# Performance work log

Measured on AMD Instinct MI355X. Metric: run time of the kernel, lower is better.

The kernel has to match this reference:

```python
import jax, jax.numpy as jnp
import numpy as np
from jax import lax

STRIDE = 16
SCALE = 16.0
ANCHOR_DIMS = (1.0, 2.0, 4.0, 8.0, 16.0, 32.0)
PRE_NMS_TOP_N = 6000
POST_NMS_TOP_N = 300
NMS_THRESH = 0.7


def conv2d(x, w, b, pad):
    y = lax.conv_general_dilated(x, w, (1, 1), [(pad, pad), (pad, pad)],
                                 dimension_numbers=("NCHW", "OIHW", "NCHW"))
    return y + b[None, :, None, None]


def setup_inputs() -> dict:
    key = jax.random.key(0)
    ks = jax.random.split(key, 6)
    B, C, H, W = 1, 1024, 128, 128
    A = len(ANCHOR_DIMS)
    return {
        "base_features": jax.random.normal(ks[0], (B, C, H, W), jnp.float32),
        "image_metadata": jnp.array([[H * STRIDE, W * STRIDE, 1.0]], jnp.float32),
        "gt_boxes": jax.random.uniform(ks[1], (B, 20, 5), jnp.float32) * 100.0,
        "W_conv": jax.random.normal(ks[2], (512, C, 3, 3), jnp.float32) / np.sqrt(C * 9.0),
        "b_conv": jnp.zeros((512,), jnp.float32),
        "W_cls": jax.random.normal(ks[3], (A, 512, 1, 1), jnp.float32) / np.sqrt(512.0),
        "b_cls": jnp.zeros((A,), jnp.float32),
        "W_bbox": jax.random.normal(ks[4], (4 * A, 512, 1, 1), jnp.float32) * 0.01,
        "b_bbox": jnp.zeros((4 * A,), jnp.float32),
    }


def _make_anchors(H, W):
    # square anchors of size dim*scale, centered on each feature cell
    dims = jnp.asarray(ANCHOR_DIMS, jnp.float32) * SCALE          # [A]
    cy = (jnp.arange(H, dtype=jnp.float32) + 0.5) * STRIDE        # [H]
    cx = (jnp.arange(W, dtype=jnp.float32) + 0.5) * STRIDE        # [W]
    half = 0.5 * dims[None, None, :]                              # [1,1,A]
    CX = cx[None, :, None]
    CY = cy[:, None, None]
    anchors = jnp.stack(jnp.broadcast_arrays(CX - half, CY - half, CX + half, CY + half), axis=-1)
    return anchors.reshape(-1, 4)                                 # [(H*W*A),4], order (h,w,a)


def _nms_fixed(boxes, scores):
    # boxes [N,4] already sorted by score desc; greedy NMS, POST_NMS_TOP_N picks
    x1, y1, x2, y2 = boxes[:, 0], boxes[:, 1], boxes[:, 2], boxes[:, 3]
    areas = jnp.maximum(x2 - x1, 0.0) * jnp.maximum(y2 - y1, 0.0)

    def body(i, state):
        alive, keep = state
        masked = jnp.where(alive, scores, -jnp.inf)
        j = jnp.argmax(masked)
        valid = masked[j] > -jnp.inf
        keep = keep.at[i].set(jnp.where(valid, j, -1).astype(jnp.int32))
        bj = boxes[j]
        iw = jnp.maximum(jnp.minimum(x2, bj[2]) - jnp.maximum(x1, bj[0]), 0.0)
        ih = jnp.maximum(jnp.minimum(y2, bj[3]) - jnp.maximum(y1, bj[1]), 0.0)
        inter = iw * ih
        iou = inter / (areas + areas[j] - inter + 1e-9)
        alive = alive & (iou <= NMS_THRESH)
        return alive, keep

    alive0 = jnp.ones(boxes.shape[0], bool)
    keep0 = jnp.full((POST_NMS_TOP_N,), -1, jnp.int32)
    _, keep = lax.fori_loop(0, POST_NMS_TOP_N, body, (alive0, keep0))
    return keep


def _proposal(prob, bbox, image_metadata):
    # original layer operates on detached tensors (.data)
    prob = lax.stop_gradient(prob)
    bbox = lax.stop_gradient(bbox)
    B, A, H, W = prob.shape
    anchors = _make_anchors(H, W)                                 # [N,4]
    scores = prob[0].transpose(1, 2, 0).reshape(-1)               # (h,w,a)
    deltas = bbox[0].reshape(A, 4, H, W).transpose(2, 3, 0, 1).reshape(-1, 4)
    wa = anchors[:, 2] - anchors[:, 0]
    ha = anchors[:, 3] - anchors[:, 1]
    cxa = anchors[:, 0] + 0.5 * wa
    cya = anchors[:, 1] + 0.5 * ha
    pcx = deltas[:, 0] * wa + cxa
    pcy = deltas[:, 1] * ha + cya
    pw = jnp.exp(deltas[:, 2]) * wa
    ph = jnp.exp(deltas[:, 3]) * ha
    boxes = jnp.stack([pcx - 0.5 * pw, pcy - 0.5 * ph, pcx + 0.5 * pw, pcy + 0.5 * ph], axis=1)
    im_h, im_w = image_metadata[0, 0], image_metadata[0, 1]
    boxes = jnp.stack([
        jnp.clip(boxes[:, 0], 0.0, im_w), jnp.clip(boxes[:, 1], 0.0, im_h),
        jnp.clip(boxes[:, 2], 0.0, im_w), jnp.clip(boxes[:, 3], 0.0, im_h)], axis=1)
    top_scores, top_idx = lax.top_k(scores, PRE_NMS_TOP_N)
    top_boxes = boxes[top_idx]
    keep = _nms_fixed(top_boxes, top_scores)
    sel = jnp.where(keep >= 0, keep, 0)
    kept = top_boxes[sel] * (keep >= 0).astype(top_boxes.dtype)[:, None]
    rois = jnp.concatenate([jnp.zeros((POST_NMS_TOP_N, 1), top_boxes.dtype), kept], axis=1)
    return rois                                                   # [POST_NMS_TOP_N, 5]


def reference(base_features, image_metadata, gt_boxes, W_conv, b_conv, W_cls, b_cls, W_bbox, b_bbox):
    conv1 = jax.nn.relu(conv2d(base_features, W_conv, b_conv, pad=1))   # [B,512,H,W]
    score = conv2d(conv1, W_cls, b_cls, pad=0)                          # [B,A,H,W]
    B, A, H, W = score.shape
    s2 = score.reshape(B, 2, (A * H) // 2, W)                           # RPN.reshape(x, 2)
    prob = jax.nn.softmax(s2, axis=1).reshape(B, A, H, W)               # reshape back to A channels
    bbox = conv2d(conv1, W_bbox, b_bbox, pad=0)                         # [B,4A,H,W]
    rois = _proposal(prob, bbox, image_metadata)
    return rois, prob, bbox
```

## Files before the change

### kernel.cpp

```cpp
#include <hip/hip_runtime.h>
#include <math.h>

typedef unsigned int u32;
typedef unsigned long long u64;
typedef short s16x8 __attribute__((ext_vector_type(8)));
typedef float f32x4 __attribute__((ext_vector_type(4)));

#define HH 128
#define WW 128
#define NPIX (128*128)
#define NANCH (NPIX*6)
#define KPRE 6000
#define KPOST 300
#define SORT_CAP 16384
#define RW 96
#define NMS_T 0.7f

#define OUT_PROB 1500
#define OUT_BBOX (1500 + 98304)

#define WS_CONV1 ((size_t)0)
#define WS_XTH   ((size_t)33554432)
#define WS_WPH   ((size_t)100663296)
#define WS_BOXES ((size_t)33554432)
#define WS_SCORE (WS_BOXES + 1572864)
#define WS_KEYS  (WS_SCORE + 393216)
#define WS_TB    (WS_KEYS + 131072)
#define WS_AREA  (WS_TB + 98304)
#define WS_SUP   (WS_AREA + 24576)
#define WS_HIST  (WS_SUP + 4718592)
#define WS_CTRL  (WS_HIST + 262144)
#define WS_KEEP  (WS_CTRL + 256)
#define WS_SKEYS (WS_KEEP + 1280)

__device__ __forceinline__ unsigned short f2bf(float x) {
    u32 b = __float_as_uint(x);
    u32 r = (b + 0x7FFFu + ((b >> 16) & 1u)) >> 16;
    return (unsigned short)r;
}

__device__ __forceinline__ void gl_lds16(const void* g, void* l) {
    __builtin_amdgcn_global_load_lds(
        (__attribute__((address_space(1))) const void*)g,
        (__attribute__((address_space(3))) void*)l,
        16, 0, 0);
}

__global__ void k_init(u32* __restrict__ hist, u32* __restrict__ ctrl,
                       int* __restrict__ keep, u64* __restrict__ keys) {
    int t = blockIdx.x * blockDim.x + threadIdx.x;
    if (t < 65536) hist[t] = 0u;
    if (t < 64)    ctrl[t] = 0u;
    if (t < 304)   keep[t] = -1;
    if (t < SORT_CAP) keys[t] = ~0ULL;
}

__global__ __launch_bounds__(256) void k_xsplit(const float* __restrict__ in,
                                                unsigned short* __restrict__ xth) {
    unsigned short* xtl = xth + 16777216;
    __shared__ unsigned short Th[64][72];
    __shared__ unsigned short Tl[64][72];
    const int px0 = blockIdx.x * 64;
    const int c0  = blockIdx.y * 64;
    const int t = threadIdx.x;
    const int r = t >> 4;
    const int p4 = (t & 15) * 4;
#pragma unroll
    for (int i = 0; i < 4; ++i) {
        int cr = r + 16 * i;
        float4 v = *(const float4*)(in + (size_t)(c0 + cr) * NPIX + px0 + p4);
        float vv[4] = {v.x, v.y, v.z, v.w};
#pragma unroll
        for (int k = 0; k < 4; ++k) {
            unsigned short h = f2bf(vv[k]);
            float hf = __uint_as_float((u32)h << 16);
            unsigned short l = f2bf(vv[k] - hf);
            Th[p4 + k][cr] = h;
            Tl[p4 + k][cr] = l;
        }
    }
    __syncthreads();
    const int p = t >> 2, q = t & 3;
    unsigned short* dh = xth + (size_t)(px0 + p) * 1024 + c0 + q * 16;
    unsigned short* dl = xtl + (size_t)(px0 + p) * 1024 + c0 + q * 16;
    *(uint4*)dh       = *(const uint4*)&Th[p][q * 16];
    *(uint4*)(dh + 8) = *(const uint4*)&Th[p][q * 16 + 8];
    *(uint4*)dl       = *(const uint4*)&Tl[p][q * 16];
    *(uint4*)(dl + 8) = *(const uint4*)&Tl[p][q * 16 + 8];
}

__global__ __launch_bounds__(256) void k_wpack(const float* __restrict__ w,
                                               unsigned short* __restrict__ wph,
                                               float* __restrict__ zstash) {
    if (blockIdx.x == 0 && threadIdx.x < 128) zstash[threadIdx.x] = 0.f;
    int id = blockIdx.x * 256 + threadIdx.x;
    int oc = id >> 10, c = id & 1023;
    const float* src = w + (size_t)oc * 9216 + c * 9;
#pragma unroll
    for (int tap = 0; tap < 9; ++tap) {
        float x = src[tap];
        unsigned short h = f2bf(x);
        unsigned short l = f2bf(x - __uint_as_float((u32)h << 16));
        wph[(size_t)tap * 524288 + id] = h;
        wph[4718592 + (size_t)tap * 524288 + id] = l;
    }
}

__global__ __launch_bounds__(256, 2) void k_conv3m(const unsigned short* __restrict__ xt,
                                                   const unsigned short* __restrict__ wp,
                                                   const float* __restrict__ bias,
                                                   const unsigned short* __restrict__ zst,
                                                   float* __restrict__ out) {
    const int ocg = blockIdx.x;
    const int y   = blockIdx.y;
    const int oc0 = ocg * 128;
    const int tid = threadIdx.x;
    const int lane = tid & 63;
    const int w    = tid >> 6;
    const int l15  = lane & 15;
    const int quad = lane >> 4;
    const int hoc  = w >> 1, hpx = w & 1;

    __shared__ __align__(16) unsigned short Lds[32768];

    const int lg  = lane & 3;
    const int lr  = lane >> 2;

    const unsigned short* xsrc[4];
    int xstep[4];
    const unsigned short* wsrc[4];

    int wp_pl[4], wp_ocr[4], wp_gs[4];
#pragma unroll
    for (int j = 0; j < 4; ++j) {
        int i = w + 4 * j;
        wp_pl[j]  = i >> 3;
        wp_ocr[j] = (i & 7) * 16 + lr;
        wp_gs[j]  = lg ^ ((wp_ocr[j] >> 1) & 3);
    }
    int xp_pl[4], xp_p[4], xp_gs[4];
#pragma unroll
    for (int j = 0; j < 4; ++j) {
        int i = w + 4 * j;
        xp_pl[j] = i >> 3;
        xp_p[j]  = (i & 7) * 16 + lr;
        xp_gs[j] = lg ^ ((xp_p[j] >> 1) & 3);
    }

    auto set_tap = [&](int tap) {
        int dy = tap / 3, dx = tap - dy * 3;
        int yy = y + dy - 1;
        bool yok = (yy >= 0) && (yy < HH);
#pragma unroll
        for (int j = 0; j < 4; ++j) {
            int x = dx - 1 + xp_p[j];
            bool ok = yok && (x >= 0) && (x < WW);
            xsrc[j] = ok ? xt + (size_t)xp_pl[j] * 16777216
                              + (size_t)(yy * WW + x) * 1024 + xp_gs[j] * 8
                         : zst + lg * 8;
            xstep[j] = ok ? 32 : 0;
        }
#pragma unroll
        for (int j = 0; j < 4; ++j)
            wsrc[j] = wp + (size_t)wp_pl[j] * 4718592 + (size_t)tap * 524288
                        + (size_t)(oc0 + wp_ocr[j]) * 1024 + wp_gs[j] * 8;
    };

    auto issue = [&](int sel) {
        const int bo = sel * 16384;
#pragma unroll
        for (int j = 0; j < 4; ++j) {
            gl_lds16(xsrc[j], &Lds[bo + (w + 4 * j) * 512]);
            xsrc[j] += xstep[j];
        }
#pragma unroll
        for (int j = 0; j < 4; ++j) {
            gl_lds16(wsrc[j], &Lds[bo + 8192 + (w + 4 * j) * 512]);
            wsrc[j] += 32;
        }
    };

    const int g  = quad ^ ((l15 >> 1) & 3);
    const int bB0 = (hpx * 64 + l15) * 32 + g * 8;
    const int bA0 = 8192 + (hoc * 64 + l15) * 32 + g * 8;

    f32x4 acc[4][4];
#pragma unroll
    for (int og = 0; og < 4; ++og)
#pragma unroll
        for (int nt = 0; nt < 4; ++nt) acc[og][nt] = (f32x4){0.f, 0.f, 0.f, 0.f};

    set_tap(0);
    issue(0);

    for (int s = 0; s < 288; ++s) {
        const int cur = s & 1;
        __syncthreads();
        if (s + 1 < 288) {
            int s1 = s + 1;
            if ((s1 & 31) == 0) set_tap(s1 >> 5);
            issue(s1 & 1);
        }

        const int bo = cur * 16384;
        s16x8 ah[4], al[4];
#pragma unroll
        for (int og = 0; og < 4; ++og) {
            ah[og] = *(const s16x8*)&Lds[bo + bA0 + og * 512];
            al[og] = *(const s16x8*)&Lds[bo + bA0 + 4096 + og * 512];
        }
#pragma unroll
        for (int nt = 0; nt < 4; ++nt) {
            const s16x8 bh = *(const s16x8*)&Lds[bo + bB0 + nt * 512];
            const s16x8 bl = *(const s16x8*)&Lds[bo + bB0 + 4096 + nt * 512];
#pragma unroll
            for (int og = 0; og < 4; ++og) {
                acc[og][nt] = __builtin_amdgcn_mfma_f32_16x16x32_bf16(ah[og], bh, acc[og][nt], 0, 0, 0);
                acc[og][nt] = __builtin_amdgcn_mfma_f32_16x16x32_bf16(ah[og], bl, acc[og][nt], 0, 0, 0);
                acc[og][nt] = __builtin_amdgcn_mfma_f32_16x16x32_bf16(al[og], bh, acc[og][nt], 0, 0, 0);
            }
        }
    }

#pragma unroll
    for (int og = 0; og < 4; ++og) {
#pragma unroll
        for (int nt = 0; nt < 4; ++nt) {
#pragma unroll
            for (int rg = 0; rg < 4; ++rg) {
                const int oc = oc0 + hoc * 64 + og * 16 + quad * 4 + rg;
                const int px = hpx * 64 + nt * 16 + l15;
                float v = acc[og][nt][rg] + bias[oc];
                out[(size_t)oc * NPIX + y * WW + px] = fmaxf(v, 0.f);
            }
        }
    }
}

__global__ __launch_bounds__(256) void k_conv1(const float* __restrict__ conv1,
                                               const float* __restrict__ wcls,
                                               const float* __restrict__ bcls,
                                               const float* __restrict__ wbox,
                                               const float* __restrict__ bboxb,
                                               float* __restrict__ out) {
    const int tid = threadIdx.x;
    const int og = tid >> 4, pg = tid & 15;
    const int px0 = blockIdx.x * 64;
    __shared__ __align__(16) float Wl[32][32];
    __shared__ __align__(16) float Xl[32][64];
    __shared__ float Sc[6][64];

    float a0[4] = {0, 0, 0, 0}, a1[4] = {0, 0, 0, 0};

    for (int cc = 0; cc < 16; ++cc) {
        {
            int u = tid;
            int row = (u * 4) >> 5;
            int col = (u * 4) & 31;
            float4 v;
            if (row < 6)       v = *(const float4*)(wcls + row * 512 + cc * 32 + col);
            else if (row < 30) v = *(const float4*)(wbox + (row - 6) * 512 + cc * 32 + col);
            else               v = make_float4(0.f, 0.f, 0.f, 0.f);
            *(float4*)&Wl[row][col] = v;
        }
        for (int u = tid; u < 512; u += 256) {
            int row = (u * 4) >> 6, col = (u * 4) & 63;
            *(float4*)&Xl[row][col] =
                *(const float4*)(conv1 + (size_t)(cc * 32 + row) * NPIX + px0 + col);
        }
        __syncthreads();
#pragma unroll
        for (int cp = 0; cp < 32; ++cp) {
            const float4 x = *(const float4*)&Xl[cp][pg * 4];
            const float w0 = Wl[og][cp];
            const float w1 = Wl[og + 16][cp];
            a0[0] = fmaf(w0, x.x, a0[0]); a0[1] = fmaf(w0, x.y, a0[1]);
            a0[2] = fmaf(w0, x.z, a0[2]); a0[3] = fmaf(w0, x.w, a0[3]);
            a1[0] = fmaf(w1, x.x, a1[0]); a1[1] = fmaf(w1, x.y, a1[1]);
            a1[2] = fmaf(w1, x.z, a1[2]); a1[3] = fmaf(w1, x.w, a1[3]);
        }
        __syncthreads();
    }
    const int pxb = px0 + pg * 4;
    if (og < 6) {
        const float bc = bcls[og];
#pragma unroll
        for (int kk = 0; kk < 4; ++kk) Sc[og][pg * 4 + kk] = a0[kk] + bc;
    } else {
        const float bb = bboxb[og - 6];
#pragma unroll
        for (int kk = 0; kk < 4; ++kk)
            out[OUT_BBOX + (size_t)(og - 6) * NPIX + pxb + kk] = a0[kk] + bb;
    }
    if (og + 16 < 30) {
        const float bb = bboxb[og + 10];
#pragma unroll
        for (int kk = 0; kk < 4; ++kk)
            out[OUT_BBOX + (size_t)(og + 10) * NPIX + pxb + kk] = a1[kk] + bb;
    }
    __syncthreads();
    if (og < 6) {
        const int pa = og < 3 ? og + 3 : og - 3;
#pragma unroll
        for (int kk = 0; kk < 4; ++kk) {
            const float s = Sc[og][pg * 4 + kk], sp = Sc[pa][pg * 4 + kk];
            out[OUT_PROB + (size_t)og * NPIX + pxb + kk] = 1.0f / (1.0f + expf(sp - s));
        }
    }
}

__global__ void k_decode(const float* __restrict__ out, const float* __restrict__ meta,
                         float4* __restrict__ boxes, float* __restrict__ scores) {
#pragma clang fp contract(off)
    int t = blockIdx.x * blockDim.x + threadIdx.x;
    if (t >= NANCH) return;
    int a = t >> 14;
    int pix = t & 16383;
    int yc = pix >> 7, xc = pix & 127;
    int n = pix * 6 + a;
    float sc = out[OUT_PROB + (size_t)a * NPIX + pix];
    float d0 = out[OUT_BBOX + (size_t)(a * 4 + 0) * NPIX + pix];
    float d1 = out[OUT_BBOX + (size_t)(a * 4 + 1) * NPIX + pix];
    float d2 = out[OUT_BBOX + (size_t)(a * 4 + 2) * NPIX + pix];
    float d3 = out[OUT_BBOX + (size_t)(a * 4 + 3) * NPIX + pix];
    const float dims = (float)(16 << a);
    const float cxa = (xc + 0.5f) * 16.f;
    const float cya = (yc + 0.5f) * 16.f;
    float pcx = d0 * dims + cxa;
    float pcy = d1 * dims + cya;
    float pw  = expf(d2) * dims;
    float ph  = expf(d3) * dims;
    float imh = meta[0], imw = meta[1];
    float x1 = fminf(fmaxf(pcx - 0.5f * pw, 0.f), imw);
    float y1 = fminf(fmaxf(pcy - 0.5f * ph, 0.f), imh);
    float x2 = fminf(fmaxf(pcx + 0.5f * pw, 0.f), imw);
    float y2 = fminf(fmaxf(pcy + 0.5f * ph, 0.f), imh);
    boxes[n] = make_float4(x1, y1, x2, y2);
    scores[n] = sc;
}

__global__ void k_hist(const float* __restrict__ scores, u32* __restrict__ hist) {
    int t = blockIdx.x * blockDim.x + threadIdx.x;
    if (t >= NANCH) return;
    u32 b = __float_as_uint(scores[t]) >> 16;
    atomicAdd(&hist[b], 1u);
}

__global__ void k_select(const u32* __restrict__ hist, u32* __restrict__ ctrl) {
    __shared__ u32 S[256];
    __shared__ u32 U[256];
    const int tid = threadIdx.x;
    u32 s = 0;
    for (int i = 0; i < 256; ++i) s += hist[tid * 256 + i];
    S[tid] = s;
    __syncthreads();
    if (tid == 0) {
        u32 acc = 0;
        for (int t2 = 255; t2 >= 0; --t2) { U[t2] = acc; acc += S[t2]; }
    }
    __syncthreads();
    if (U[tid] < KPRE && U[tid] + S[tid] >= KPRE) {
        u32 acc = U[tid];
        for (int b = tid * 256 + 255; b >= tid * 256; --b) {
            u32 h = hist[b];
            if (acc + h >= KPRE) { ctrl[1] = (u32)b; ctrl[2] = acc; break; }
            acc += h;
        }
    }
}

__global__ void k_compact(const float* __restrict__ scores, u32* __restrict__ ctrl,
                          u64* __restrict__ keys) {
    int t = blockIdx.x * blockDim.x + threadIdx.x;
    if (t >= NANCH) return;
    u32 bits = __float_as_uint(scores[t]);
    if ((bits >> 16) >= ctrl[1]) {
        u32 pos = atomicAdd(&ctrl[0], 1u);
        if (pos < SORT_CAP) keys[pos] = ((u64)(~bits) << 32) | (u32)t;
    }
}

__global__ __launch_bounds__(1024) void k_sort_local(u64* __restrict__ keys) {
    __shared__ u64 lds[8192];
    const int tid = threadIdx.x;
    u64* g = keys + blockIdx.x * 8192;
    for (int u = tid; u < 8192; u += 1024) lds[u] = g[u];
    __syncthreads();
    for (int k = 2; k <= 8192; k <<= 1) {
        for (int j = k >> 1; j > 0; j >>= 1) {
            for (int u = tid; u < 4096; u += 1024) {
                int i = ((u & ~(j - 1)) << 1) | (u & (j - 1));
                int l = i | j;
                bool up = (i & k) == 0;
                u64 x = lds[i], y2 = lds[l];
                if ((x > y2) == up) { lds[i] = y2; lds[l] = x; }
            }
            __syncthreads();
        }
    }
    for (int u = tid; u < 8192; u += 1024) g[u] = lds[u];
}

__global__ void k_merge(const u64* __restrict__ keys, u64* __restrict__ skeys) {
    int i = blockIdx.x * blockDim.x + threadIdx.x;
    if (i >= KPRE) return;
    const u64* A = keys;
    const u64* B = keys + 8192;
    int lo = i > 8192 ? i - 8192 : 0;
    int hi = i < 8192 ? i : 8192;
    while (lo < hi) {
        int a = (lo + hi) >> 1;
        if (A[a] < B[i - a - 1]) lo = a + 1; else hi = a;
    }
    int a = lo, b = i - lo;
    u64 va = (a < 8192) ? A[a] : ~0ULL;
    u64 vb = (b < 8192) ? B[b] : ~0ULL;
    skeys[i] = va < vb ? va : vb;
}

__global__ void k_gather(const u64* __restrict__ skeys, const float4* __restrict__ boxes,
                         float4* __restrict__ tb, float* __restrict__ areas) {
#pragma clang fp contract(off)
    int i = blockIdx.x * blockDim.x + threadIdx.x;
    if (i >= KPRE) return;
    u32 n = (u32)(skeys[i] & 0xFFFFFFFFULL);
    float4 b = boxes[n];
    tb[i] = b;
    areas[i] = fmaxf(b.z - b.x, 0.f) * fmaxf(b.w - b.y, 0.f);
}

__global__ __launch_bounds__(256) void k_bitmap(const float4* __restrict__ tb,
                                                const float* __restrict__ areas,
                                                u64* __restrict__ suppr) {
#pragma clang fp contract(off)
    const int i = blockIdx.x;
    const int lane = threadIdx.x & 63;
    const int wv = threadIdx.x >> 6;
    const float4 bi = tb[i];
    const float ai = areas[i];
    for (int Wd = wv; Wd < RW; Wd += 4) {
        int j = Wd * 64 + lane;
        bool sup = false;
        if (j < KPRE) {
            float4 bj = tb[j];
            float iw = fmaxf(fminf(bi.z, bj.z) - fmaxf(bi.x, bj.x), 0.f);
            float ih = fmaxf(fminf(bi.w, bj.w) - fmaxf(bi.y, bj.y), 0.f);
            float inter = iw * ih;
            float denom = ((areas[j] + ai) - inter) + 1e-9f;
            sup = (inter / denom) > NMS_T;
        }
        u64 m = __ballot(sup);
        if (lane == 0) suppr[(size_t)i * RW + Wd] = m;
    }
}

__global__ void k_scan(const u64* __restrict__ suppr, int* __restrict__ keep) {
    const int lane = threadIdx.x;
    u64 a0 = (lane < 93) ? ~0ULL : (lane == 93 ? ((1ULL << 48) - 1) : 0ULL);
    const int w1 = lane + 64;
    u64 a1 = (w1 < 93) ? ~0ULL : (w1 == 93 ? ((1ULL << 48) - 1) : 0ULL);
    int kept = 0;
    int i = 0;
    while (kept < KPOST) {
        int wi = i >> 6;
        if (wi >= 94) break;
        u64 wvv = (wi < 64) ? __shfl(a0, wi) : __shfl(a1, wi - 64);
        wvv &= (~0ULL) << (i & 63);
        if (wvv == 0ULL) { i = (wi + 1) << 6; continue; }
        int b = __ffsll((long long)wvv) - 1;
        i = (wi << 6) + b;
        if (lane == 0) keep[kept] = i;
        kept++;
        const u64* row = suppr + (size_t)i * RW;
        u64 s0 = row[lane];
        u64 s1 = (lane + 64 < RW) ? row[lane + 64] : 0ULL;
        a0 &= ~s0;
        a1 &= ~s1;
        i++;
    }
}

__global__ void k_rois(const int* __restrict__ keep, const float4* __restrict__ tb,
                       float* __restrict__ out) {
    int r = blockIdx.x * blockDim.x + threadIdx.x;
    if (r >= KPOST) return;
    int k = keep[r];
    float4 b = make_float4(0.f, 0.f, 0.f, 0.f);
    if (k >= 0) b = tb[k];
    out[r * 5 + 0] = 0.f;
    out[r * 5 + 1] = b.x;
    out[r * 5 + 2] = b.y;
    out[r * 5 + 3] = b.z;
    out[r * 5 + 4] = b.w;
}

extern "C" void kernel_launch(void* const* d_in, const int* in_sizes, int n_in,
                              void* d_out, int out_size, void* d_ws, size_t ws_size,
                              hipStream_t stream) {
    (void)in_sizes; (void)n_in; (void)out_size; (void)ws_size;
    const float* x     = (const float*)d_in[0];
    const float* meta  = (const float*)d_in[1];
    const float* wc3   = (const float*)d_in[3];
    const float* bc3   = (const float*)d_in[4];
    const float* wcls  = (const float*)d_in[5];
    const float* bcls  = (const float*)d_in[6];
    const float* wbox  = (const float*)d_in[7];
    const float* bboxb = (const float*)d_in[8];
    float* out = (float*)d_out;
    char* ws = (char*)d_ws;

    float*  conv1  = (float*)(ws + WS_CONV1);
    float4* boxes  = (float4*)(ws + WS_BOXES);
    float*  scores = (float*)(ws + WS_SCORE);
    u64*    keys   = (u64*)(ws + WS_KEYS);
    float4* tb     = (float4*)(ws + WS_TB);
    float*  areas  = (float*)(ws + WS_AREA);
    u64*    suppr  = (u64*)(ws + WS_SUP);
    u32*    hist   = (u32*)(ws + WS_HIST);
    u32*    ctrl   = (u32*)(ws + WS_CTRL);
    int*    keep   = (int*)(ws + WS_KEEP);
    u64*    skeys  = (u64*)(ws + WS_SKEYS);

    float* zstash = out;

    unsigned short* xth = (unsigned short*)(ws + WS_XTH);
    unsigned short* wph = (unsigned short*)(ws + WS_WPH);
    k_xsplit<<<dim3(256, 16), 256, 0, stream>>>(x, xth);
    k_wpack<<<2048, 256, 0, stream>>>(wc3, wph, zstash);
    k_conv3m<<<dim3(4, 128), 256, 0, stream>>>(xth, wph, bc3,
                                               (const unsigned short*)zstash, conv1);

    k_init<<<256, 256, 0, stream>>>(hist, ctrl, keep, keys);
    k_conv1<<<256, 256, 0, stream>>>(conv1, wcls, bcls, wbox, bboxb, out);
    k_decode<<<384, 256, 0, stream>>>(out, meta, boxes, scores);
    k_hist<<<384, 256, 0, stream>>>(scores, hist);
    k_select<<<1, 256, 0, stream>>>(hist, ctrl);
    k_compact<<<384, 256, 0, stream>>>(scores, ctrl, keys);
    k_sort_local<<<2, 1024, 0, stream>>>(keys);
    k_merge<<<24, 256, 0, stream>>>(keys, skeys);
    k_gather<<<24, 256, 0, stream>>>(skeys, boxes, tb, areas);
    k_bitmap<<<6000, 256, 0, stream>>>(tb, areas, suppr);
    k_scan<<<1, 64, 0, stream>>>(suppr, keep);
    k_rois<<<2, 256, 0, stream>>>(keep, tb, out);
}
```

Before: 928.1 us.

## Restructure conv3 into per-wave pipelines; fuse hist, parallelize select, prefetch NMS scan

The 3x3 conv kernel now uses 128-thread blocks in which each wave owns a private LDS double buffer, tracks its own loads with explicit waitcnt instead of block barriers, and prefetches the next stage's fragments into registers while running the current MFMAs. The grid gains a z dimension that splits the row into two pixel halves. The histogram atomic is folded into k_decode, and top-k threshold selection is split into a parallel group reduction and a single-block refine step. The NMS scan prefetches the next candidate's suppression row to hide load latency, at the cost of more registers and more complex control flow.

```diff
diff --git a/kernel.cpp b/kernel.cpp
--- a/kernel.cpp
+++ b/kernel.cpp
@@ -32,6 +32,11 @@
 #define WS_CTRL  (WS_HIST + 262144)
 #define WS_KEEP  (WS_CTRL + 256)
 #define WS_SKEYS (WS_KEEP + 1280)
+#define WS_GSUM  (WS_SKEYS + 49152)
+
+#define WC_VM16  0x4F70
+#define WC_VM0   0x0F70
+#define WC_LGKM0 0xC07F
 
 __device__ __forceinline__ unsigned short f2bf(float x) {
     u32 b = __float_as_uint(x);
@@ -106,135 +111,140 @@
     }
 }
 
-__global__ __launch_bounds__(256, 2) void k_conv3m(const unsigned short* __restrict__ xt,
+struct Frags { s16x8 ah[4], al[4], bh[4], bl[4]; };
+
+__global__ __launch_bounds__(128, 1) void k_conv3m(const unsigned short* __restrict__ xt,
                                                    const unsigned short* __restrict__ wp,
                                                    const float* __restrict__ bias,
                                                    const unsigned short* __restrict__ zst,
                                                    float* __restrict__ out) {
     const int ocg = blockIdx.x;
     const int y   = blockIdx.y;
-    const int oc0 = ocg * 128;
+    const int xh  = blockIdx.z;
     const int tid = threadIdx.x;
     const int lane = tid & 63;
     const int w    = tid >> 6;
     const int l15  = lane & 15;
     const int quad = lane >> 4;
-    const int hoc  = w >> 1, hpx = w & 1;
+    const int oc0w = ocg * 128 + w * 64;
+    const int px0w = xh * 64;
 
     __shared__ __align__(16) unsigned short Lds[32768];
-
+    unsigned short* WB = &Lds[w * 16384];
+
+    const int lr  = lane >> 2;
     const int lg  = lane & 3;
-    const int lr  = lane >> 2;
-
-    const unsigned short* xsrc[4];
-    int xstep[4];
-    const unsigned short* wsrc[4];
-
-    int wp_pl[4], wp_ocr[4], wp_gs[4];
-#pragma unroll
-    for (int j = 0; j < 4; ++j) {
-        int i = w + 4 * j;
-        wp_pl[j]  = i >> 3;
-        wp_ocr[j] = (i & 7) * 16 + lr;
-        wp_gs[j]  = lg ^ ((wp_ocr[j] >> 1) & 3);
-    }
-    int xp_pl[4], xp_p[4], xp_gs[4];
-#pragma unroll
-    for (int j = 0; j < 4; ++j) {
-        int i = w + 4 * j;
-        xp_pl[j] = i >> 3;
-        xp_p[j]  = (i & 7) * 16 + lr;
-        xp_gs[j] = lg ^ ((xp_p[j] >> 1) & 3);
-    }
+    const int csw = lg ^ ((lr >> 1) & 3);
+
+    const unsigned short* src[16];
+    int step[16];
 
     auto set_tap = [&](int tap) {
-        int dy = tap / 3, dx = tap - dy * 3;
-        int yy = y + dy - 1;
-        bool yok = (yy >= 0) && (yy < HH);
-#pragma unroll
-        for (int j = 0; j < 4; ++j) {
-            int x = dx - 1 + xp_p[j];
-            bool ok = yok && (x >= 0) && (x < WW);
-            xsrc[j] = ok ? xt + (size_t)xp_pl[j] * 16777216
-                              + (size_t)(yy * WW + x) * 1024 + xp_gs[j] * 8
+        const int dy = tap / 3, dx = tap - dy * 3;
+        const int yy = y + dy - 1;
+        const bool yok = (yy >= 0) && (yy < HH);
+#pragma unroll
+        for (int j = 0; j < 8; ++j) {
+            const int pl  = j >> 2;
+            const int row = (j & 3) * 16 + lr;
+            src[j]  = wp + (size_t)pl * 4718592 + (size_t)tap * 524288
+                         + (size_t)(oc0w + row) * 1024 + csw * 8;
+            step[j] = 32;
+        }
+#pragma unroll
+        for (int j = 8; j < 16; ++j) {
+            const int pl = (j >> 2) & 1;
+            const int p  = (j & 3) * 16 + lr;
+            const int x  = px0w - 1 + dx + p;
+            const bool ok = yok && (x >= 0) && (x < WW);
+            src[j]  = ok ? xt + (size_t)pl * 16777216
+                              + (size_t)(yy * WW + x) * 1024 + csw * 8
                          : zst + lg * 8;
-            xstep[j] = ok ? 32 : 0;
-        }
-#pragma unroll
-        for (int j = 0; j < 4; ++j)
-            wsrc[j] = wp + (size_t)wp_pl[j] * 4718592 + (size_t)tap * 524288
-                        + (size_t)(oc0 + wp_ocr[j]) * 1024 + wp_gs[j] * 8;
+            step[j] = ok ? 32 : 0;
+        }
     };
 
-    auto issue = [&](int sel) {
-        const int bo = sel * 16384;
-#pragma unroll
-        for (int j = 0; j < 4; ++j) {
-            gl_lds16(xsrc[j], &Lds[bo + (w + 4 * j) * 512]);
-            xsrc[j] += xstep[j];
-        }
-#pragma unroll
-        for (int j = 0; j < 4; ++j) {
-            gl_lds16(wsrc[j], &Lds[bo + 8192 + (w + 4 * j) * 512]);
-            wsrc[j] += 32;
+    auto issue = [&](int buf) {
+        unsigned short* db = WB + buf * 8192;
+#pragma unroll
+        for (int j = 0; j < 16; ++j) {
+            gl_lds16(src[j], db + j * 512);
+            src[j] += step[j];
         }
     };
 
     const int g  = quad ^ ((l15 >> 1) & 3);
-    const int bB0 = (hpx * 64 + l15) * 32 + g * 8;
-    const int bA0 = 8192 + (hoc * 64 + l15) * 32 + g * 8;
+    const int ra = l15 * 32 + g * 8;
+
+    auto readf = [&](Frags& F, const unsigned short* rb) {
+#pragma unroll
+        for (int og = 0; og < 4; ++og) {
+            F.ah[og] = *(const s16x8*)&rb[ra + og * 512];
+            F.al[og] = *(const s16x8*)&rb[ra + 2048 + og * 512];
+        }
+#pragma unroll
+        for (int nt = 0; nt < 4; ++nt) {
+            F.bh[nt] = *(const s16x8*)&rb[ra + 4096 + nt * 512];
+            F.bl[nt] = *(const s16x8*)&rb[ra + 6144 + nt * 512];
+        }
+    };
 
     f32x4 acc[4][4];
 #pragma unroll
     for (int og = 0; og < 4; ++og)
 #pragma unroll
         for (int nt = 0; nt < 4; ++nt) acc[og][nt] = (f32x4){0.f, 0.f, 0.f, 0.f};
+
+    auto domfma = [&](Frags& F) {
+#pragma unroll
+        for (int nt = 0; nt < 4; ++nt)
+#pragma unroll
+            for (int og = 0; og < 4; ++og) {
+                acc[og][nt] = __builtin_amdgcn_mfma_f32_16x16x32_bf16(F.ah[og], F.bh[nt], acc[og][nt], 0, 0, 0);
+                acc[og][nt] = __builtin_amdgcn_mfma_f32_16x16x32_bf16(F.ah[og], F.bl[nt], acc[og][nt], 0, 0, 0);
+                acc[og][nt] = __builtin_amdgcn_mfma_f32_16x16x32_bf16(F.al[og], F.bh[nt], acc[og][nt], 0, 0, 0);
+            }
+    };
+
+    Frags FA, FB;
+
+    auto stage = [&](int s, Frags& Fc, Frags& Fn) {
+        const int cur = s & 1;
+        __builtin_amdgcn_s_waitcnt(WC_LGKM0);
+        if (s + 2 < 288) {
+            if (((s + 2) & 31) == 0) set_tap((s + 2) >> 5);
+            issue(cur);
+            __builtin_amdgcn_s_waitcnt(WC_VM16);
+        } else {
+            __builtin_amdgcn_s_waitcnt(WC_VM0);
+        }
+        if (s + 1 < 288) readf(Fn, WB + (cur ^ 1) * 8192);
+        domfma(Fc);
+    };
 
     set_tap(0);
     issue(0);
-
-    for (int s = 0; s < 288; ++s) {
-        const int cur = s & 1;
-        __syncthreads();
-        if (s + 1 < 288) {
-            int s1 = s + 1;
-            if ((s1 & 31) == 0) set_tap(s1 >> 5);
-            issue(s1 & 1);
-        }
-
-        const int bo = cur * 16384;
-        s16x8 ah[4], al[4];
-#pragma unroll
-        for (int og = 0; og < 4; ++og) {
-            ah[og] = *(const s16x8*)&Lds[bo + bA0 + og * 512];
-            al[og] = *(const s16x8*)&Lds[bo + bA0 + 4096 + og * 512];
-        }
-#pragma unroll
-        for (int nt = 0; nt < 4; ++nt) {
-            const s16x8 bh = *(const s16x8*)&Lds[bo + bB0 + nt * 512];
-            const s16x8 bl = *(const s16x8*)&Lds[bo + bB0 + 4096 + nt * 512];
-#pragma unroll
-            for (int og = 0; og < 4; ++og) {
-                acc[og][nt] = __builtin_amdgcn_mfma_f32_16x16x32_bf16(ah[og], bh, acc[og][nt], 0, 0, 0);
-                acc[og][nt] = __builtin_amdgcn_mfma_f32_16x16x32_bf16(ah[og], bl, acc[og][nt], 0, 0, 0);
-                acc[og][nt] = __builtin_amdgcn_mfma_f32_16x16x32_bf16(al[og], bh, acc[og][nt], 0, 0, 0);
-            }
-        }
-    }
-
-#pragma unroll
-    for (int og = 0; og < 4; ++og) {
-#pragma unroll
-        for (int nt = 0; nt < 4; ++nt) {
+    issue(1);
+    __builtin_amdgcn_s_waitcnt(WC_VM16);
+    readf(FA, WB);
+
+#pragma unroll 1
+    for (int sp = 0; sp < 144; ++sp) {
+        stage(2 * sp,     FA, FB);
+        stage(2 * sp + 1, FB, FA);
+    }
+
+#pragma unroll
+    for (int og = 0; og < 4; ++og)
+#pragma unroll
+        for (int nt = 0; nt < 4; ++nt)
 #pragma unroll
             for (int rg = 0; rg < 4; ++rg) {
-                const int oc = oc0 + hoc * 64 + og * 16 + quad * 4 + rg;
-                const int px = hpx * 64 + nt * 16 + l15;
+                const int oc = oc0w + og * 16 + quad * 4 + rg;
+                const int px = px0w + nt * 16 + l15;
                 float v = acc[og][nt][rg] + bias[oc];
                 out[(size_t)oc * NPIX + y * WW + px] = fmaxf(v, 0.f);
             }
-        }
-    }
 }
 
 __global__ __launch_bounds__(256) void k_conv1(const float* __restrict__ conv1,
@@ -310,7 +320,8 @@
 }
 
 __global__ void k_decode(const float* __restrict__ out, const float* __restrict__ meta,
-                         float4* __restrict__ boxes, float* __restrict__ scores) {
+                         float4* __restrict__ boxes, float* __restrict__ scores,
+                         u32* __restrict__ hist) {
 #pragma clang fp contract(off)
     int t = blockIdx.x * blockDim.x + threadIdx.x;
     if (t >= NANCH) return;
@@ -337,33 +348,46 @@
     float y2 = fminf(fmaxf(pcy + 0.5f * ph, 0.f), imh);
     boxes[n] = make_float4(x1, y1, x2, y2);
     scores[n] = sc;
-}
-
-__global__ void k_hist(const float* __restrict__ scores, u32* __restrict__ hist) {
-    int t = blockIdx.x * blockDim.x + threadIdx.x;
-    if (t >= NANCH) return;
-    u32 b = __float_as_uint(scores[t]) >> 16;
-    atomicAdd(&hist[b], 1u);
-}
-
-__global__ void k_select(const u32* __restrict__ hist, u32* __restrict__ ctrl) {
+    atomicAdd(&hist[__float_as_uint(sc) >> 16], 1u);
+}
+
+__global__ __launch_bounds__(256) void k_select1(const u32* __restrict__ hist,
+                                                 u32* __restrict__ gsum) {
+    __shared__ u32 red[256];
+    const int t = threadIdx.x;
+    red[t] = hist[blockIdx.x * 256 + t];
+    __syncthreads();
+    for (int s = 128; s > 0; s >>= 1) {
+        if (t < s) red[t] += red[t + s];
+        __syncthreads();
+    }
+    if (t == 0) gsum[blockIdx.x] = red[0];
+}
+
+__global__ void k_select2(const u32* __restrict__ hist, const u32* __restrict__ gsum,
+                          u32* __restrict__ ctrl) {
     __shared__ u32 S[256];
     __shared__ u32 U[256];
-    const int tid = threadIdx.x;
-    u32 s = 0;
-    for (int i = 0; i < 256; ++i) s += hist[tid * 256 + i];
-    S[tid] = s;
-    __syncthreads();
-    if (tid == 0) {
+    __shared__ u32 Hh[256];
+    __shared__ int gsel;
+    const int t = threadIdx.x;
+    S[t] = gsum[t];
+    __syncthreads();
+    if (t == 0) {
         u32 acc = 0;
-        for (int t2 = 255; t2 >= 0; --t2) { U[t2] = acc; acc += S[t2]; }
-    }
-    __syncthreads();
-    if (U[tid] < KPRE && U[tid] + S[tid] >= KPRE) {
-        u32 acc = U[tid];
-        for (int b = tid * 256 + 255; b >= tid * 256; --b) {
-            u32 h = hist[b];
-            if (acc + h >= KPRE) { ctrl[1] = (u32)b; ctrl[2] = acc; break; }
+        for (int g2 = 255; g2 >= 0; --g2) { U[g2] = acc; acc += S[g2]; }
+    }
+    __syncthreads();
+    if (U[t] < KPRE && U[t] + S[t] >= KPRE) gsel = t;
+    __syncthreads();
+    const int g = gsel;
+    Hh[t] = hist[g * 256 + t];
+    __syncthreads();
+    if (t == 0) {
+        u32 acc = U[g];
+        for (int b2 = 255; b2 >= 0; --b2) {
+            u32 h = Hh[b2];
+            if (acc + h >= KPRE) { ctrl[1] = (u32)(g * 256 + b2); ctrl[2] = acc; break; }
             acc += h;
         }
     }
@@ -459,24 +483,42 @@
     u64 a0 = (lane < 93) ? ~0ULL : (lane == 93 ? ((1ULL << 48) - 1) : 0ULL);
     const int w1 = lane + 64;
     u64 a1 = (w1 < 93) ? ~0ULL : (w1 == 93 ? ((1ULL << 48) - 1) : 0ULL);
+
+    auto nexta = [&](int i) -> int {
+        int p = i + 1;
+        int wi = p >> 6, off = p & 63;
+        while (wi < 94) {
+            u64 wv = (wi < 64) ? __shfl(a0, wi) : __shfl(a1, wi - 64);
+            wv &= (~0ULL) << off;
+            if (wv) return (wi << 6) + __ffsll((long long)wv) - 1;
+            ++wi; off = 0;
+        }
+        return -1;
+    };
+
+    int i = 0;
+    u64 r0 = suppr[lane];
+    u64 r1 = (lane + 64 < RW) ? suppr[lane + 64] : 0ULL;
     int kept = 0;
-    int i = 0;
-    while (kept < KPOST) {
-        int wi = i >> 6;
-        if (wi >= 94) break;
-        u64 wvv = (wi < 64) ? __shfl(a0, wi) : __shfl(a1, wi - 64);
-        wvv &= (~0ULL) << (i & 63);
-        if (wvv == 0ULL) { i = (wi + 1) << 6; continue; }
-        int b = __ffsll((long long)wvv) - 1;
-        i = (wi << 6) + b;
+    while (true) {
         if (lane == 0) keep[kept] = i;
         kept++;
-        const u64* row = suppr + (size_t)i * RW;
-        u64 s0 = row[lane];
-        u64 s1 = (lane + 64 < RW) ? row[lane + 64] : 0ULL;
-        a0 &= ~s0;
-        a1 &= ~s1;
-        i++;
+        if (kept >= KPOST) break;
+        int i2 = nexta(i);
+        u64 p0 = 0, p1 = 0;
+        if (i2 >= 0) {
+            p0 = suppr[(size_t)i2 * RW + lane];
+            p1 = (lane + 64 < RW) ? suppr[(size_t)i2 * RW + lane + 64] : 0ULL;
+        }
+        a0 &= ~r0; a1 &= ~r1;
+        int j = nexta(i);
+        if (j < 0) break;
+        if (j == i2) { r0 = p0; r1 = p1; }
+        else {
+            r0 = suppr[(size_t)j * RW + lane];
+            r1 = (lane + 64 < RW) ? suppr[(size_t)j * RW + lane + 64] : 0ULL;
+        }
+        i = j;
     }
 }
 
@@ -520,6 +562,7 @@
     u32*    ctrl   = (u32*)(ws + WS_CTRL);
     int*    keep   = (int*)(ws + WS_KEEP);
     u64*    skeys  = (u64*)(ws + WS_SKEYS);
+    u32*    gsum   = (u32*)(ws + WS_GSUM);
 
     float* zstash = out;
 
@@ -527,14 +570,14 @@
     unsigned short* wph = (unsigned short*)(ws + WS_WPH);
     k_xsplit<<<dim3(256, 16), 256, 0, stream>>>(x, xth);
     k_wpack<<<2048, 256, 0, stream>>>(wc3, wph, zstash);
-    k_conv3m<<<dim3(4, 128), 256, 0, stream>>>(xth, wph, bc3,
-                                               (const unsigned short*)zstash, conv1);
+    k_conv3m<<<dim3(4, 128, 2), 128, 0, stream>>>(xth, wph, bc3,
+                                                  (const unsigned short*)zstash, conv1);
 
     k_init<<<256, 256, 0, stream>>>(hist, ctrl, keep, keys);
     k_conv1<<<256, 256, 0, stream>>>(conv1, wcls, bcls, wbox, bboxb, out);
-    k_decode<<<384, 256, 0, stream>>>(out, meta, boxes, scores);
-    k_hist<<<384, 256, 0, stream>>>(scores, hist);
-    k_select<<<1, 256, 0, stream>>>(hist, ctrl);
+    k_decode<<<384, 256, 0, stream>>>(out, meta, boxes, scores, hist);
+    k_select1<<<256, 256, 0, stream>>>(hist, gsum);
+    k_select2<<<1, 256, 0, stream>>>(hist, gsum, ctrl);
     k_compact<<<384, 256, 0, stream>>>(scores, ctrl, keys);
     k_sort_local<<<2, 1024, 0, stream>>>(keys);
     k_merge<<<24, 256, 0, stream>>>(keys, skeys);
```

Measured after the change: 1.137 ms. 22.6% more time.
